# Optimization experiments

Measured on AMD Instinct MI355X. Metric: run time of the kernel, lower is better.

## Reference

```python
import jax, jax.numpy as jnp
import numpy as np

EPS = 1e-5


def _bn(a, gamma, beta):
    # training-mode BatchNorm1d applied independently at each timestep:
    # statistics over the batch axis (axis=1) of a [T, B, H] tensor (biased var).
    mu = a.mean(axis=1, keepdims=True)
    var = a.var(axis=1, keepdims=True)
    return gamma * (a - mu) * jax.lax.rsqrt(var + EPS) + beta


def _layer(x, W_xz, b_xz, g_z, beta_z, W_hz, b_hz, W_xh, b_xh, g_h, beta_h, W_hh, b_hh):
    # Precompute the input-side projections + BN for all timesteps (one big GEMM),
    # then scan only the recurrent part.
    az = _bn(jnp.einsum('tbi,hi->tbh', x, W_xz) + b_xz, g_z, beta_z)  # [T,B,H]
    ah = _bn(jnp.einsum('tbi,hi->tbh', x, W_xh) + b_xh, g_h, beta_h)  # [T,B,H]
    B = x.shape[1]
    H = W_hz.shape[0]

    def step(h, inp):
        az_t, ah_t = inp
        Z = jax.nn.sigmoid(az_t + h @ W_hz.T + b_hz)
        Ht = jax.nn.relu(ah_t + h @ W_hh.T + b_hh)
        h2 = Z * h + (1.0 - Z) * Ht
        return h2, h2

    h0 = jnp.zeros((B, H), x.dtype)
    _, ys = jax.lax.scan(step, h0, (az, ah))
    return ys  # [T,B,H]


def setup_inputs() -> dict:
    key = jax.random.key(0)
    T, B, I, H = 500, 64, 512, 1024
    ks = iter(jax.random.split(key, 24))

    def rn(shape, fan):
        return jax.random.normal(next(ks), shape, jnp.float32) / np.sqrt(fan)

    d = {"x": jax.random.normal(next(ks), (T, B, I), jnp.float32)}
    for l, fin in enumerate([I, H]):
        d[f"W_xz{l}"] = rn((H, fin), fin)
        d[f"b_xz{l}"] = rn((H,), fin)
        d[f"g_z{l}"] = jnp.ones((H,), jnp.float32)
        d[f"beta_z{l}"] = jnp.zeros((H,), jnp.float32)
        d[f"W_hz{l}"] = rn((H, H), H)
        d[f"b_hz{l}"] = rn((H,), H)
        d[f"W_xh{l}"] = rn((H, fin), fin)
        d[f"b_xh{l}"] = rn((H,), fin)
        d[f"g_h{l}"] = jnp.ones((H,), jnp.float32)
        d[f"beta_h{l}"] = jnp.zeros((H,), jnp.float32)
        d[f"W_hh{l}"] = rn((H, H), H)
        d[f"b_hh{l}"] = rn((H,), H)
    return d


def reference(x,
              W_xz0, b_xz0, g_z0, beta_z0, W_hz0, b_hz0, W_xh0, b_xh0, g_h0, beta_h0, W_hh0, b_hh0,
              W_xz1, b_xz1, g_z1, beta_z1, W_hz1, b_hz1, W_xh1, b_xh1, g_h1, beta_h1, W_hh1, b_hh1):
    h = _layer(x, W_xz0, b_xz0, g_z0, beta_z0, W_hz0, b_hz0,
               W_xh0, b_xh0, g_h0, beta_h0, W_hh0, b_hh0)
    h = _layer(h, W_xz1, b_xz1, g_z1, beta_z1, W_hz1, b_hz1,
               W_xh1, b_xh1, g_h1, beta_h1, W_hh1, b_hh1)
    return h  # [T, B, hidden_size]
```

## Files before the change

### kernel.cpp

```cpp
#include <hip/hip_runtime.h>

#define TT 500
#define NB_BATCH 64
#define HID 1024
#define NC 2048

typedef __attribute__((ext_vector_type(8))) __bf16 bf16x8;
typedef __attribute__((ext_vector_type(8))) unsigned short us8;
typedef __attribute__((ext_vector_type(4))) unsigned short us4;
typedef __attribute__((ext_vector_type(4))) float f32x4;
typedef __attribute__((ext_vector_type(2))) unsigned long long u64x2;

__device__ __forceinline__ unsigned short f2bf(float f) {
  unsigned u = __builtin_bit_cast(unsigned, f);
  u += 0x7fffu + ((u >> 16) & 1u);
  return (unsigned short)(u >> 16);
}
__device__ __forceinline__ float bf2f(unsigned short h) {
  unsigned u = ((unsigned)h) << 16;
  return __builtin_bit_cast(float, u);
}
__device__ __forceinline__ bf16x8 ld_bf8(const unsigned short* p) {
  return __builtin_bit_cast(bf16x8, *(const us8*)p);
}

__global__ __launch_bounds__(256) void conv_f32_bf16(
    const float* __restrict__ src, unsigned short* __restrict__ dst)
{
  int i = blockIdx.x * 256 + threadIdx.x;
  const float4* s = (const float4*)src + (size_t)i * 2;
  float4 a = s[0], b = s[1];
  us8 o;
  o[0] = f2bf(a.x); o[1] = f2bf(a.y); o[2] = f2bf(a.z); o[3] = f2bf(a.w);
  o[4] = f2bf(b.x); o[5] = f2bf(b.y); o[6] = f2bf(b.z); o[7] = f2bf(b.w);
  *((us8*)dst + i) = o;
}

#define XS_STR 40
#define WS_STR 40

__global__ __launch_bounds__(256) void proj_bn_kernel(
    const unsigned short* __restrict__ X, int K,
    const unsigned short* __restrict__ Wxz, const unsigned short* __restrict__ Wxh,
    const float* __restrict__ gz, const float* __restrict__ bz,
    const float* __restrict__ gh, const float* __restrict__ bh,
    unsigned short* __restrict__ A)
{
  __shared__ unsigned short Xs[64 * XS_STR];
  __shared__ unsigned short Ws[256 * WS_STR];

  const int t   = blockIdx.x >> 3;
  const int nt  = blockIdx.x & 7;
  const int tid = threadIdx.x;
  const int wave = tid >> 6;
  const int lane = tid & 63;
  const int lm = lane & 15;
  const int lq = lane >> 4;

  const unsigned short* Wsrc = (nt < 4) ? (Wxz + (size_t)(nt * 256) * K)
                                        : (Wxh + (size_t)((nt - 4) * 256) * K);
  const unsigned short* Xbase = X + (size_t)(t * 64) * K;

  f32x4 acc[4][4];
#pragma unroll
  for (int i = 0; i < 4; i++)
#pragma unroll
    for (int j = 0; j < 4; j++) acc[i][j] = (f32x4){0.f, 0.f, 0.f, 0.f};

  const int nkt = K >> 5;
  for (int kt = 0; kt < nkt; ++kt) {
    const int k0 = kt << 5;
#pragma unroll
    for (int it = 0; it < 2; ++it) {
      int idx = it * 256 + tid;
      int r = idx >> 3, c4 = idx & 7;
      *(us4*)&Xs[r * XS_STR + c4 * 4] =
          *(const us4*)(Xbase + (size_t)r * K + k0 + c4 * 4);
    }
#pragma unroll
    for (int it = 0; it < 8; ++it) {
      int idx = it * 256 + tid;
      int r = idx >> 3, c4 = idx & 7;
      *(us4*)&Ws[r * WS_STR + c4 * 4] =
          *(const us4*)(Wsrc + (size_t)r * K + k0 + c4 * 4);
    }
    __syncthreads();
    bf16x8 bfr[4];
#pragma unroll
    for (int j = 0; j < 4; ++j)
      bfr[j] = ld_bf8(&Ws[(wave * 64 + j * 16 + lm) * WS_STR + lq * 8]);
#pragma unroll
    for (int rt = 0; rt < 4; ++rt) {
      bf16x8 afr = ld_bf8(&Xs[(rt * 16 + lm) * XS_STR + lq * 8]);
#pragma unroll
      for (int j = 0; j < 4; ++j)
        acc[rt][j] = __builtin_amdgcn_mfma_f32_16x16x32_bf16(afr, bfr[j], acc[rt][j], 0, 0, 0);
    }
    __syncthreads();
  }

  const float inv64 = 1.0f / 64.0f;
#pragma unroll
  for (int ct = 0; ct < 4; ++ct) {
    float s1 = 0.f, s2 = 0.f;
#pragma unroll
    for (int rt = 0; rt < 4; ++rt)
#pragma unroll
      for (int r = 0; r < 4; ++r) {
        float v = acc[rt][ct][r];
        s1 += v; s2 += v * v;
      }
    s1 += __shfl_xor(s1, 16, 64); s2 += __shfl_xor(s2, 16, 64);
    s1 += __shfl_xor(s1, 32, 64); s2 += __shfl_xor(s2, 32, 64);
    float mean = s1 * inv64;
    float var  = s2 * inv64 - mean * mean;
    int col = nt * 256 + wave * 64 + ct * 16 + lm;
    float g, be;
    if (col < 1024) { g = gz[col];        be = bz[col]; }
    else            { g = gh[col - 1024]; be = bh[col - 1024]; }
    float scale = g * rsqrtf(var + 1e-5f);
    float shift = be - mean * scale;
    unsigned short* Aout = A + (size_t)(t * 64) * NC + col;
#pragma unroll
    for (int rt = 0; rt < 4; ++rt)
#pragma unroll
      for (int r = 0; r < 4; ++r) {
        int b = rt * 16 + lq * 4 + r;
        Aout[(size_t)b * NC] = f2bf(acc[rt][ct][r] * scale + shift);
      }
  }
}

__global__ __launch_bounds__(64) void scan_kernel(
    const unsigned short* __restrict__ A,
    const float* __restrict__ Whz, const float* __restrict__ bhz,
    const float* __restrict__ Whh, const float* __restrict__ bhh,
    unsigned short* __restrict__ hbuf,
    float* __restrict__ ys,
    unsigned* __restrict__ flags,
    const int ysfmt)
{
  extern __shared__ unsigned short Wlds[];
  const int lane = threadIdx.x;
  const int fg = blockIdx.x & 63;
  const int bg = blockIdx.x >> 6;
  const int lm = lane & 15;
  const int lq = lane >> 4;
  const int jg = fg * 16 + lm;

  for (int g = 0; g < 2; ++g) {
    const float* Wsrc = (g ? Whh : Whz) + (size_t)(fg * 16) * HID;
#pragma unroll 4
    for (int it = 0; it < 64; ++it) {
      int idx = it * 64 + lane;
      int r = idx >> 8, c4 = idx & 255;
      float4 v = *(const float4*)(Wsrc + (size_t)r * HID + c4 * 4);
      int c = c4 >> 1, hh = c4 & 1;
      us4 o; o[0] = f2bf(v.x); o[1] = f2bf(v.y); o[2] = f2bf(v.z); o[3] = f2bf(v.w);
      *(us4*)&Wlds[g * 16384 + r * 1024 + (((c + 5 * r) & 127) << 3) + hh * 4] = o;
    }
  }
  const float bzv = bhz[jg];
  const float bhv = bhh[jg];
  __syncthreads();

  unsigned short aznx[4], ahnx[4];
  {
    const unsigned short* p = A + (size_t)(bg * 16 + lq * 4) * NC + jg;
#pragma unroll
    for (int r = 0; r < 4; ++r) { aznx[r] = p[(size_t)r * NC]; ahnx[r] = p[(size_t)r * NC + 1024]; }
  }
  float h_own[4] = {0.f, 0.f, 0.f, 0.f};

  unsigned* myflag   = &flags[blockIdx.x * 16];
  unsigned* pollflag = &flags[(bg * 64 + lane) * 16];

  for (int t = 0; t < TT; ++t) {
    f32x4 azp[4], ahp[4];
#pragma unroll
    for (int j = 0; j < 4; ++j) {
      azp[j] = (f32x4){0.f, 0.f, 0.f, 0.f};
      ahp[j] = (f32x4){0.f, 0.f, 0.f, 0.f};
    }

    unsigned short azc[4], ahc[4];
#pragma unroll
    for (int r = 0; r < 4; ++r) { azc[r] = aznx[r]; ahc[r] = ahnx[r]; }
    if (t + 1 < TT) {
      const unsigned short* p = A + ((size_t)(t + 1) * 64 + bg * 16 + lq * 4) * NC + jg;
#pragma unroll
      for (int r = 0; r < 4; ++r) { aznx[r] = p[(size_t)r * NC]; ahnx[r] = p[(size_t)r * NC + 1024]; }
    }

    if (t > 0) {
      const unsigned tv = (unsigned)t;
      unsigned v = __hip_atomic_load(pollflag, __ATOMIC_RELAXED, __HIP_MEMORY_SCOPE_AGENT);
      while (__ballot(v < tv)) {
        __builtin_amdgcn_s_sleep(1);
        v = __hip_atomic_load(pollflag, __ATOMIC_RELAXED, __HIP_MEMORY_SCOPE_AGENT);
      }
      __atomic_signal_fence(__ATOMIC_SEQ_CST);

      const unsigned long long* hq = (const unsigned long long*)
          (hbuf + (size_t)(t & 1) * 65536 + (size_t)(bg * 16 + lm) * HID) + lq * 2;
      unsigned long long harr[64];
#pragma unroll
      for (int kt = 0; kt < 32; ++kt) {
        harr[2 * kt]     = __hip_atomic_load(hq + kt * 8,     __ATOMIC_RELAXED, __HIP_MEMORY_SCOPE_AGENT);
        harr[2 * kt + 1] = __hip_atomic_load(hq + kt * 8 + 1, __ATOMIC_RELAXED, __HIP_MEMORY_SCOPE_AGENT);
      }
#pragma unroll
      for (int kt = 0; kt < 32; ++kt) {
        u64x2 u; u[0] = harr[2 * kt]; u[1] = harr[2 * kt + 1];
        bf16x8 afr = __builtin_bit_cast(bf16x8, u);
        int c = ((kt * 4 + lq) + 5 * lm) & 127;
        bf16x8 bz8 = ld_bf8(&Wlds[lm * 1024 + c * 8]);
        bf16x8 bh8 = ld_bf8(&Wlds[16384 + lm * 1024 + c * 8]);
        azp[kt & 3] = __builtin_amdgcn_mfma_f32_16x16x32_bf16(afr, bz8, azp[kt & 3], 0, 0, 0);
        ahp[kt & 3] = __builtin_amdgcn_mfma_f32_16x16x32_bf16(afr, bh8, ahp[kt & 3], 0, 0, 0);
      }
    }

    f32x4 accz = (azp[0] + azp[1]) + (azp[2] + azp[3]);
    f32x4 acch = (ahp[0] + ahp[1]) + (ahp[2] + ahp[3]);

    unsigned short* hb = hbuf + (size_t)((t + 1) & 1) * 65536;
    unsigned short mybf[4];
#pragma unroll
    for (int r = 0; r < 4; ++r) {
      float z  = 1.0f / (1.0f + __expf(-(bf2f(azc[r]) + accz[r] + bzv)));
      float ht = bf2f(ahc[r]) + acch[r] + bhv;
      ht = ht > 0.f ? ht : 0.f;
      float h2 = z * h_own[r] + (1.0f - z) * ht;
      h_own[r] = h2;
      mybf[r] = f2bf(h2);
    }
#pragma unroll
    for (int r = 0; r < 4; ++r) {
      int p = __shfl((int)mybf[r], lane ^ 1, 64);
      if (!(lane & 1)) {
        unsigned w = (unsigned)mybf[r] | ((unsigned)p << 16);
        int row = bg * 16 + lq * 4 + r;
        __hip_atomic_store((unsigned*)(hb + (size_t)row * HID + jg), w,
                           __ATOMIC_RELAXED, __HIP_MEMORY_SCOPE_AGENT);
      }
    }

    __atomic_signal_fence(__ATOMIC_SEQ_CST);
    __builtin_amdgcn_s_waitcnt(0);
    __atomic_signal_fence(__ATOMIC_SEQ_CST);
    if (lane == 0)
      __hip_atomic_store(myflag, (unsigned)(t + 1), __ATOMIC_RELAXED, __HIP_MEMORY_SCOPE_AGENT);

    if (ysfmt) {
      float* ysp = ys + ((size_t)t * 64 + bg * 16 + lq * 4) * HID + jg;
#pragma unroll
      for (int r = 0; r < 4; ++r) ysp[(size_t)r * HID] = h_own[r];
    } else {
      unsigned short* yb = (unsigned short*)ys +
          ((size_t)t * 64 + bg * 16 + lq * 4) * HID + jg;
#pragma unroll
      for (int r = 0; r < 4; ++r) {
        int p = __shfl((int)mybf[r], lane ^ 1, 64);
        if (!(lane & 1)) {
          unsigned w = (unsigned)mybf[r] | ((unsigned)p << 16);
          *(unsigned*)(yb + (size_t)r * HID) = w;
        }
      }
    }
  }
}

extern "C" void kernel_launch(void* const* d_in, const int* in_sizes, int n_in,
                              void* d_out, int out_size, void* d_ws, size_t ws_size,
                              hipStream_t stream)
{
  (void)in_sizes; (void)n_in; (void)out_size; (void)ws_size;
  const float* x    = (const float*)d_in[0];
  const float* Wxz0 = (const float*)d_in[1];
  const float* gz0  = (const float*)d_in[3];
  const float* bz0  = (const float*)d_in[4];
  const float* Whz0 = (const float*)d_in[5];
  const float* bhz0 = (const float*)d_in[6];
  const float* Wxh0 = (const float*)d_in[7];
  const float* gh0  = (const float*)d_in[9];
  const float* bh0  = (const float*)d_in[10];
  const float* Whh0 = (const float*)d_in[11];
  const float* bhh0 = (const float*)d_in[12];
  const float* Wxz1 = (const float*)d_in[13];
  const float* gz1  = (const float*)d_in[15];
  const float* bz1  = (const float*)d_in[16];
  const float* Whz1 = (const float*)d_in[17];
  const float* bhz1 = (const float*)d_in[18];
  const float* Wxh1 = (const float*)d_in[19];
  const float* gh1  = (const float*)d_in[21];
  const float* bh1  = (const float*)d_in[22];
  const float* Whh1 = (const float*)d_in[23];
  const float* bhh1 = (const float*)d_in[24];

  char* ws = (char*)d_ws;
  unsigned* flags0 = (unsigned*)(ws);
  unsigned* flags1 = (unsigned*)(ws + 32768);
  unsigned short* hbuf  = (unsigned short*)(ws + 65536);
  unsigned short* A     = (unsigned short*)(ws + 524288);
  unsigned short* ys0bf = (unsigned short*)(ws + 131596288);
  unsigned short* Xbf   = (unsigned short*)(ws + 197132288);
  unsigned short* Wzbf  = (unsigned short*)(ws + 229900288);
  unsigned short* Whbf  = (unsigned short*)(ws + 231997440);
  float* out = (float*)d_out;

  hipMemsetAsync(ws, 0, 65536, stream);

  conv_f32_bf16<<<dim3(8000), dim3(256), 0, stream>>>(x, Xbf);
  conv_f32_bf16<<<dim3(256),  dim3(256), 0, stream>>>(Wxz0, Wzbf);
  conv_f32_bf16<<<dim3(256),  dim3(256), 0, stream>>>(Wxh0, Whbf);

  proj_bn_kernel<<<dim3(4000), dim3(256), 0, stream>>>(
      Xbf, 512, Wzbf, Whbf, gz0, bz0, gh0, bh0, A);
  {
    const unsigned short* a0 = A;
    const float* whz = Whz0; const float* vbz = bhz0;
    const float* whh = Whh0; const float* vbh = bhh0;
    unsigned short* hb = hbuf; float* yy = (float*)ys0bf; unsigned* ff = flags0;
    int fmt = 0;
    void* kargs[9] = {&a0, &whz, &vbz, &whh, &vbh, &hb, &yy, &ff, &fmt};
    hipLaunchCooperativeKernel((const void*)scan_kernel, dim3(256), dim3(64),
                               kargs, 65536, stream);
  }

  conv_f32_bf16<<<dim3(512), dim3(256), 0, stream>>>(Wxz1, Wzbf);
  conv_f32_bf16<<<dim3(512), dim3(256), 0, stream>>>(Wxh1, Whbf);

  proj_bn_kernel<<<dim3(4000), dim3(256), 0, stream>>>(
      ys0bf, 1024, Wzbf, Whbf, gz1, bz1, gh1, bh1, A);
  {
    const unsigned short* a0 = A;
    const float* whz = Whz1; const float* vbz = bhz1;
    const float* whh = Whh1; const float* vbh = bhh1;
    unsigned short* hb = hbuf; float* yy = out; unsigned* ff = flags1;
    int fmt = 1;
    void* kargs[9] = {&a0, &whz, &vbz, &whh, &vbh, &hb, &yy, &ff, &fmt};
    hipLaunchCooperativeKernel((const void*)scan_kernel, dim3(256), dim3(64),
                               kargs, 65536, stream);
  }
}
```

Baseline: 4.746 ms.

## Fuse layer-1 input projection into layer-0 scan and defer BN to layer-1 scan

The layer-0 scan now reuses each loaded h_{t-1} tile to also compute the layer-1 input projection (W_xz1, W_xh1) with MFMA. It writes raw bf16 pre-BN activations plus per-batch-group partial sum and sum-of-squares stats. The layer-1 scan then applies BatchNorm on the fly from those stats, which removes the separate second proj_bn GEMM kernel and the ys0 round-trip. In exchange, each layer-0 step does double the MFMA work and reads W1 from global memory (not LDS) inside the serial critical loop. Variance is computed as E[x²]-mean² from bf16-era sums, and the 4-way split accumulators are collapsed into single accumulators, which lengthens the MFMA dependency chains.

After: 5.953 ms. 25.4% more time.

```diff
diff --git a/kernel.cpp b/kernel.cpp
--- a/kernel.cpp
+++ b/kernel.cpp
@@ -22,6 +22,20 @@
 }
 __device__ __forceinline__ bf16x8 ld_bf8(const unsigned short* p) {
   return __builtin_bit_cast(bf16x8, *(const us8*)p);
+}
+
+__device__ __forceinline__ void bn_coeff(const float* __restrict__ stats,
+                                         int t, int col, float g, float be,
+                                         float& sc, float& sh) {
+  const float* sb = stats + ((size_t)t * 2048 + col) * 8;
+  float4 q0 = *(const float4*)sb;
+  float4 q1 = *(const float4*)(sb + 4);
+  float s1 = q0.x + q0.z + q1.x + q1.z;
+  float s2 = q0.y + q0.w + q1.y + q1.w;
+  float mean = s1 * (1.0f / 64.0f);
+  float var  = s2 * (1.0f / 64.0f) - mean * mean;
+  sc = g * rsqrtf(var + 1e-5f);
+  sh = be - mean * sc;
 }
 
 __global__ __launch_bounds__(256) void conv_f32_bf16(
@@ -131,14 +145,16 @@
   }
 }
 
-__global__ __launch_bounds__(64) void scan_kernel(
+__global__ __launch_bounds__(64) void scan0_kernel(
     const unsigned short* __restrict__ A,
     const float* __restrict__ Whz, const float* __restrict__ bhz,
     const float* __restrict__ Whh, const float* __restrict__ bhh,
     unsigned short* __restrict__ hbuf,
-    float* __restrict__ ys,
     unsigned* __restrict__ flags,
-    const int ysfmt)
+    const unsigned short* __restrict__ W1xz,
+    const unsigned short* __restrict__ W1xh,
+    unsigned short* __restrict__ rawA1,
+    float* __restrict__ stats)
 {
   extern __shared__ unsigned short Wlds[];
   const int lane = threadIdx.x;
@@ -164,6 +180,9 @@
   const float bhv = bhh[jg];
   __syncthreads();
 
+  const unsigned short* w1zr = W1xz + (size_t)jg * HID + lq * 8;
+  const unsigned short* w1hr = W1xh + (size_t)jg * HID + lq * 8;
+
   unsigned short aznx[4], ahnx[4];
   {
     const unsigned short* p = A + (size_t)(bg * 16 + lq * 4) * NC + jg;
@@ -175,21 +194,19 @@
   unsigned* myflag   = &flags[blockIdx.x * 16];
   unsigned* pollflag = &flags[(bg * 64 + lane) * 16];
 
-  for (int t = 0; t < TT; ++t) {
-    f32x4 azp[4], ahp[4];
-#pragma unroll
-    for (int j = 0; j < 4; ++j) {
-      azp[j] = (f32x4){0.f, 0.f, 0.f, 0.f};
-      ahp[j] = (f32x4){0.f, 0.f, 0.f, 0.f};
-    }
+  for (int t = 0; t <= TT; ++t) {
+    f32x4 accz = {0.f, 0.f, 0.f, 0.f}, acch = {0.f, 0.f, 0.f, 0.f};
+    unsigned long long harr[64];
 
     unsigned short azc[4], ahc[4];
-#pragma unroll
-    for (int r = 0; r < 4; ++r) { azc[r] = aznx[r]; ahc[r] = ahnx[r]; }
-    if (t + 1 < TT) {
-      const unsigned short* p = A + ((size_t)(t + 1) * 64 + bg * 16 + lq * 4) * NC + jg;
-#pragma unroll
-      for (int r = 0; r < 4; ++r) { aznx[r] = p[(size_t)r * NC]; ahnx[r] = p[(size_t)r * NC + 1024]; }
+    if (t < TT) {
+#pragma unroll
+      for (int r = 0; r < 4; ++r) { azc[r] = aznx[r]; ahc[r] = ahnx[r]; }
+      if (t + 1 < TT) {
+        const unsigned short* p = A + ((size_t)(t + 1) * 64 + bg * 16 + lq * 4) * NC + jg;
+#pragma unroll
+        for (int r = 0; r < 4; ++r) { aznx[r] = p[(size_t)r * NC]; ahnx[r] = p[(size_t)r * NC + 1024]; }
+      }
     }
 
     if (t > 0) {
@@ -203,6 +220,176 @@
 
       const unsigned long long* hq = (const unsigned long long*)
           (hbuf + (size_t)(t & 1) * 65536 + (size_t)(bg * 16 + lm) * HID) + lq * 2;
+#pragma unroll
+      for (int kt = 0; kt < 32; ++kt) {
+        harr[2 * kt]     = __hip_atomic_load(hq + kt * 8,     __ATOMIC_RELAXED, __HIP_MEMORY_SCOPE_AGENT);
+        harr[2 * kt + 1] = __hip_atomic_load(hq + kt * 8 + 1, __ATOMIC_RELAXED, __HIP_MEMORY_SCOPE_AGENT);
+      }
+      if (t < TT) {
+#pragma unroll
+        for (int kt = 0; kt < 32; ++kt) {
+          u64x2 u; u[0] = harr[2 * kt]; u[1] = harr[2 * kt + 1];
+          bf16x8 afr = __builtin_bit_cast(bf16x8, u);
+          int c = ((kt * 4 + lq) + 5 * lm) & 127;
+          bf16x8 bz8 = ld_bf8(&Wlds[lm * 1024 + c * 8]);
+          bf16x8 bh8 = ld_bf8(&Wlds[16384 + lm * 1024 + c * 8]);
+          accz = __builtin_amdgcn_mfma_f32_16x16x32_bf16(afr, bz8, accz, 0, 0, 0);
+          acch = __builtin_amdgcn_mfma_f32_16x16x32_bf16(afr, bh8, acch, 0, 0, 0);
+        }
+      }
+    }
+
+    if (t < TT) {
+      unsigned short* hb = hbuf + (size_t)((t + 1) & 1) * 65536;
+      unsigned short mybf[4];
+#pragma unroll
+      for (int r = 0; r < 4; ++r) {
+        float z  = 1.0f / (1.0f + __expf(-(bf2f(azc[r]) + accz[r] + bzv)));
+        float ht = bf2f(ahc[r]) + acch[r] + bhv;
+        ht = ht > 0.f ? ht : 0.f;
+        float h2 = z * h_own[r] + (1.0f - z) * ht;
+        h_own[r] = h2;
+        mybf[r] = f2bf(h2);
+      }
+#pragma unroll
+      for (int r = 0; r < 4; ++r) {
+        int p = __shfl((int)mybf[r], lane ^ 1, 64);
+        if (!(lane & 1)) {
+          unsigned w = (unsigned)mybf[r] | ((unsigned)p << 16);
+          int row = bg * 16 + lq * 4 + r;
+          __hip_atomic_store((unsigned*)(hb + (size_t)row * HID + jg), w,
+                             __ATOMIC_RELAXED, __HIP_MEMORY_SCOPE_AGENT);
+        }
+      }
+
+      __atomic_signal_fence(__ATOMIC_SEQ_CST);
+      __builtin_amdgcn_s_waitcnt(0);
+      __atomic_signal_fence(__ATOMIC_SEQ_CST);
+      if (lane == 0)
+        __hip_atomic_store(myflag, (unsigned)(t + 1), __ATOMIC_RELAXED, __HIP_MEMORY_SCOPE_AGENT);
+    }
+
+    if (t > 0) {
+      f32x4 a1z = {0.f, 0.f, 0.f, 0.f}, a1h = {0.f, 0.f, 0.f, 0.f};
+#pragma unroll
+      for (int kt = 0; kt < 32; ++kt) {
+        u64x2 u; u[0] = harr[2 * kt]; u[1] = harr[2 * kt + 1];
+        bf16x8 afr = __builtin_bit_cast(bf16x8, u);
+        bf16x8 bz8 = ld_bf8(w1zr + kt * 32);
+        bf16x8 bh8 = ld_bf8(w1hr + kt * 32);
+        a1z = __builtin_amdgcn_mfma_f32_16x16x32_bf16(afr, bz8, a1z, 0, 0, 0);
+        a1h = __builtin_amdgcn_mfma_f32_16x16x32_bf16(afr, bh8, a1h, 0, 0, 0);
+      }
+      float s1z = 0.f, s2z = 0.f, s1h = 0.f, s2h = 0.f;
+#pragma unroll
+      for (int r = 0; r < 4; ++r) {
+        s1z += a1z[r]; s2z += a1z[r] * a1z[r];
+        s1h += a1h[r]; s2h += a1h[r] * a1h[r];
+      }
+      s1z += __shfl_xor(s1z, 16, 64); s2z += __shfl_xor(s2z, 16, 64);
+      s1z += __shfl_xor(s1z, 32, 64); s2z += __shfl_xor(s2z, 32, 64);
+      s1h += __shfl_xor(s1h, 16, 64); s2h += __shfl_xor(s2h, 16, 64);
+      s1h += __shfl_xor(s1h, 32, 64); s2h += __shfl_xor(s2h, 32, 64);
+      const size_t t1 = (size_t)(t - 1);
+      if (lq == 0) {
+        *(float2*)(stats + ((t1 * 2048 + jg) * 4 + bg) * 2)        = make_float2(s1z, s2z);
+        *(float2*)(stats + ((t1 * 2048 + jg + 1024) * 4 + bg) * 2) = make_float2(s1h, s2h);
+      }
+      unsigned short a1zbf[4], a1hbf[4];
+#pragma unroll
+      for (int r = 0; r < 4; ++r) { a1zbf[r] = f2bf(a1z[r]); a1hbf[r] = f2bf(a1h[r]); }
+#pragma unroll
+      for (int r = 0; r < 4; ++r) {
+        int pz = __shfl((int)a1zbf[r], lane ^ 1, 64);
+        int ph = __shfl((int)a1hbf[r], lane ^ 1, 64);
+        if (!(lane & 1)) {
+          int row = bg * 16 + lq * 4 + r;
+          unsigned short* rp = rawA1 + (t1 * 64 + row) * NC + jg;
+          *(unsigned*)rp          = (unsigned)a1zbf[r] | ((unsigned)pz << 16);
+          *(unsigned*)(rp + 1024) = (unsigned)a1hbf[r] | ((unsigned)ph << 16);
+        }
+      }
+    }
+  }
+}
+
+__global__ __launch_bounds__(64) void scan1_kernel(
+    const unsigned short* __restrict__ rawA1,
+    const float* __restrict__ stats,
+    const float* __restrict__ g_z, const float* __restrict__ be_z,
+    const float* __restrict__ g_h, const float* __restrict__ be_h,
+    const float* __restrict__ Whz, const float* __restrict__ bhz,
+    const float* __restrict__ Whh, const float* __restrict__ bhh,
+    unsigned short* __restrict__ hbuf,
+    unsigned* __restrict__ flags,
+    float* __restrict__ ys)
+{
+  extern __shared__ unsigned short Wlds[];
+  const int lane = threadIdx.x;
+  const int fg = blockIdx.x & 63;
+  const int bg = blockIdx.x >> 6;
+  const int lm = lane & 15;
+  const int lq = lane >> 4;
+  const int jg = fg * 16 + lm;
+
+  for (int g = 0; g < 2; ++g) {
+    const float* Wsrc = (g ? Whh : Whz) + (size_t)(fg * 16) * HID;
+#pragma unroll 4
+    for (int it = 0; it < 64; ++it) {
+      int idx = it * 64 + lane;
+      int r = idx >> 8, c4 = idx & 255;
+      float4 v = *(const float4*)(Wsrc + (size_t)r * HID + c4 * 4);
+      int c = c4 >> 1, hh = c4 & 1;
+      us4 o; o[0] = f2bf(v.x); o[1] = f2bf(v.y); o[2] = f2bf(v.z); o[3] = f2bf(v.w);
+      *(us4*)&Wlds[g * 16384 + r * 1024 + (((c + 5 * r) & 127) << 3) + hh * 4] = o;
+    }
+  }
+  const float bzv = bhz[jg];
+  const float bhv = bhh[jg];
+  const float gzv = g_z[jg],  bezv = be_z[jg];
+  const float ghv = g_h[jg],  behv = be_h[jg];
+  __syncthreads();
+
+  unsigned short aznx[4], ahnx[4];
+  float sczn, shzn, schn, shhn;
+  {
+    const unsigned short* p = rawA1 + (size_t)(bg * 16 + lq * 4) * NC + jg;
+#pragma unroll
+    for (int r = 0; r < 4; ++r) { aznx[r] = p[(size_t)r * NC]; ahnx[r] = p[(size_t)r * NC + 1024]; }
+    bn_coeff(stats, 0, jg,        gzv, bezv, sczn, shzn);
+    bn_coeff(stats, 0, jg + 1024, ghv, behv, schn, shhn);
+  }
+  float h_own[4] = {0.f, 0.f, 0.f, 0.f};
+
+  unsigned* myflag   = &flags[blockIdx.x * 16];
+  unsigned* pollflag = &flags[(bg * 64 + lane) * 16];
+
+  for (int t = 0; t < TT; ++t) {
+    f32x4 accz = {0.f, 0.f, 0.f, 0.f}, acch = {0.f, 0.f, 0.f, 0.f};
+
+    unsigned short azc[4], ahc[4];
+    float sczc = sczn, shzc = shzn, schc = schn, shhc = shhn;
+#pragma unroll
+    for (int r = 0; r < 4; ++r) { azc[r] = aznx[r]; ahc[r] = ahnx[r]; }
+    if (t + 1 < TT) {
+      const unsigned short* p = rawA1 + ((size_t)(t + 1) * 64 + bg * 16 + lq * 4) * NC + jg;
+#pragma unroll
+      for (int r = 0; r < 4; ++r) { aznx[r] = p[(size_t)r * NC]; ahnx[r] = p[(size_t)r * NC + 1024]; }
+      bn_coeff(stats, t + 1, jg,        gzv, bezv, sczn, shzn);
+      bn_coeff(stats, t + 1, jg + 1024, ghv, behv, schn, shhn);
+    }
+
+    if (t > 0) {
+      const unsigned tv = (unsigned)t;
+      unsigned v = __hip_atomic_load(pollflag, __ATOMIC_RELAXED, __HIP_MEMORY_SCOPE_AGENT);
+      while (__ballot(v < tv)) {
+        __builtin_amdgcn_s_sleep(1);
+        v = __hip_atomic_load(pollflag, __ATOMIC_RELAXED, __HIP_MEMORY_SCOPE_AGENT);
+      }
+      __atomic_signal_fence(__ATOMIC_SEQ_CST);
+
+      const unsigned long long* hq = (const unsigned long long*)
+          (hbuf + (size_t)(t & 1) * 65536 + (size_t)(bg * 16 + lm) * HID) + lq * 2;
       unsigned long long harr[64];
 #pragma unroll
       for (int kt = 0; kt < 32; ++kt) {
@@ -216,20 +403,19 @@
         int c = ((kt * 4 + lq) + 5 * lm) & 127;
         bf16x8 bz8 = ld_bf8(&Wlds[lm * 1024 + c * 8]);
         bf16x8 bh8 = ld_bf8(&Wlds[16384 + lm * 1024 + c * 8]);
-        azp[kt & 3] = __builtin_amdgcn_mfma_f32_16x16x32_bf16(afr, bz8, azp[kt & 3], 0, 0, 0);
-        ahp[kt & 3] = __builtin_amdgcn_mfma_f32_16x16x32_bf16(afr, bh8, ahp[kt & 3], 0, 0, 0);
-      }
-    }
-
-    f32x4 accz = (azp[0] + azp[1]) + (azp[2] + azp[3]);
-    f32x4 acch = (ahp[0] + ahp[1]) + (ahp[2] + ahp[3]);
+        accz = __builtin_amdgcn_mfma_f32_16x16x32_bf16(afr, bz8, accz, 0, 0, 0);
+        acch = __builtin_amdgcn_mfma_f32_16x16x32_bf16(afr, bh8, acch, 0, 0, 0);
+      }
+    }
 
     unsigned short* hb = hbuf + (size_t)((t + 1) & 1) * 65536;
     unsigned short mybf[4];
 #pragma unroll
     for (int r = 0; r < 4; ++r) {
-      float z  = 1.0f / (1.0f + __expf(-(bf2f(azc[r]) + accz[r] + bzv)));
-      float ht = bf2f(ahc[r]) + acch[r] + bhv;
+      float az = bf2f(azc[r]) * sczc + shzc;
+      float ah = bf2f(ahc[r]) * schc + shhc;
+      float z  = 1.0f / (1.0f + __expf(-(az + accz[r] + bzv)));
+      float ht = ah + acch[r] + bhv;
       ht = ht > 0.f ? ht : 0.f;
       float h2 = z * h_own[r] + (1.0f - z) * ht;
       h_own[r] = h2;
@@ -252,22 +438,9 @@
     if (lane == 0)
       __hip_atomic_store(myflag, (unsigned)(t + 1), __ATOMIC_RELAXED, __HIP_MEMORY_SCOPE_AGENT);
 
-    if (ysfmt) {
-      float* ysp = ys + ((size_t)t * 64 + bg * 16 + lq * 4) * HID + jg;
-#pragma unroll
-      for (int r = 0; r < 4; ++r) ysp[(size_t)r * HID] = h_own[r];
-    } else {
-      unsigned short* yb = (unsigned short*)ys +
-          ((size_t)t * 64 + bg * 16 + lq * 4) * HID + jg;
-#pragma unroll
-      for (int r = 0; r < 4; ++r) {
-        int p = __shfl((int)mybf[r], lane ^ 1, 64);
-        if (!(lane & 1)) {
-          unsigned w = (unsigned)mybf[r] | ((unsigned)p << 16);
-          *(unsigned*)(yb + (size_t)r * HID) = w;
-        }
-      }
-    }
+    float* ysp = ys + ((size_t)t * 64 + bg * 16 + lq * 4) * HID + jg;
+#pragma unroll
+    for (int r = 0; r < 4; ++r) ysp[(size_t)r * HID] = h_own[r];
   }
 }
 
@@ -302,45 +475,50 @@
   unsigned* flags0 = (unsigned*)(ws);
   unsigned* flags1 = (unsigned*)(ws + 32768);
   unsigned short* hbuf  = (unsigned short*)(ws + 65536);
-  unsigned short* A     = (unsigned short*)(ws + 524288);
-  unsigned short* ys0bf = (unsigned short*)(ws + 131596288);
-  unsigned short* Xbf   = (unsigned short*)(ws + 197132288);
-  unsigned short* Wzbf  = (unsigned short*)(ws + 229900288);
-  unsigned short* Whbf  = (unsigned short*)(ws + 231997440);
+  unsigned short* rawA1 = (unsigned short*)(ws + 524288);
+  float* stats          = (float*)(ws + 131596288);
+  unsigned short* Xbf   = (unsigned short*)(ws + 164364288);
+  unsigned short* Wz0bf = (unsigned short*)(ws + 197132288);
+  unsigned short* Wh0bf = (unsigned short*)(ws + 198180864);
+  unsigned short* Wz1bf = (unsigned short*)(ws + 199229440);
+  unsigned short* Wh1bf = (unsigned short*)(ws + 201326592);
+  unsigned short* A0 = (unsigned short*)d_out;
   float* out = (float*)d_out;
 
   hipMemsetAsync(ws, 0, 65536, stream);
 
   conv_f32_bf16<<<dim3(8000), dim3(256), 0, stream>>>(x, Xbf);
-  conv_f32_bf16<<<dim3(256),  dim3(256), 0, stream>>>(Wxz0, Wzbf);
-  conv_f32_bf16<<<dim3(256),  dim3(256), 0, stream>>>(Wxh0, Whbf);
+  conv_f32_bf16<<<dim3(256),  dim3(256), 0, stream>>>(Wxz0, Wz0bf);
+  conv_f32_bf16<<<dim3(256),  dim3(256), 0, stream>>>(Wxh0, Wh0bf);
+  conv_f32_bf16<<<dim3(512),  dim3(256), 0, stream>>>(Wxz1, Wz1bf);
+  conv_f32_bf16<<<dim3(512),  dim3(256), 0, stream>>>(Wxh1, Wh1bf);
 
   proj_bn_kernel<<<dim3(4000), dim3(256), 0, stream>>>(
-      Xbf, 512, Wzbf, Whbf, gz0, bz0, gh0, bh0, A);
+      Xbf, 512, Wz0bf, Wh0bf, gz0, bz0, gh0, bh0, A0);
+
   {
-    const unsigned short* a0 = A;
+    const unsigned short* a0 = A0;
     const float* whz = Whz0; const float* vbz = bhz0;
     const float* whh = Whh0; const float* vbh = bhh0;
-    unsigned short* hb = hbuf; float* yy = (float*)ys0bf; unsigned* ff = flags0;
-    int fmt = 0;
-    void* kargs[9] = {&a0, &whz, &vbz, &whh, &vbh, &hb, &yy, &ff, &fmt};
-    hipLaunchCooperativeKernel((const void*)scan_kernel, dim3(256), dim3(64),
+    unsigned short* hb = hbuf; unsigned* ff = flags0;
+    const unsigned short* w1z = Wz1bf; const unsigned short* w1h = Wh1bf;
+    unsigned short* ra = rawA1; float* st = stats;
+    void* kargs[11] = {&a0, &whz, &vbz, &whh, &vbh, &hb, &ff, &w1z, &w1h, &ra, &st};
+    hipLaunchCooperativeKernel((const void*)scan0_kernel, dim3(256), dim3(64),
                                kargs, 65536, stream);
   }
 
-  conv_f32_bf16<<<dim3(512), dim3(256), 0, stream>>>(Wxz1, Wzbf);
-  conv_f32_bf16<<<dim3(512), dim3(256), 0, stream>>>(Wxh1, Whbf);
-
-  proj_bn_kernel<<<dim3(4000), dim3(256), 0, stream>>>(
-      ys0bf, 1024, Wzbf, Whbf, gz1, bz1, gh1, bh1, A);
   {
-    const unsigned short* a0 = A;
+    const unsigned short* ra = rawA1; const float* st = stats;
+    const float* gz = gz1; const float* bez = bz1;
+    const float* gh = gh1; const float* beh = bh1;
     const float* whz = Whz1; const float* vbz = bhz1;
     const float* whh = Whh1; const float* vbh = bhh1;
-    unsigned short* hb = hbuf; float* yy = out; unsigned* ff = flags1;
-    int fmt = 1;
-    void* kargs[9] = {&a0, &whz, &vbz, &whh, &vbh, &hb, &yy, &ff, &fmt};
-    hipLaunchCooperativeKernel((const void*)scan_kernel, dim3(256), dim3(64),
+    unsigned short* hb = hbuf; unsigned* ff = flags1;
+    float* yy = out;
+    void* kargs[13] = {&ra, &st, &gz, &bez, &gh, &beh,
+                       &whz, &vbz, &whh, &vbh, &hb, &ff, &yy};
+    hipLaunchCooperativeKernel((const void*)scan1_kernel, dim3(256), dim3(64),
                                kargs, 65536, stream);
   }
 }
```
